# Performance work log

Hardware: AMD Instinct MI355X
Metric: run time of the kernel (lower is better)

Reference implementation:

```python
import math
import jax, jax.numpy as jnp
import numpy as np

DIM = 1024
HID = 2048  # int(dim * expansion_factor)
QK = 128
G = 256     # group size
B, N = 4, 4096
NUM_BUCKETS = 32
MAX_DIST = 128


def _rel_pos_bias(rel_emb, g, scale):
    # non-causal T5 relative position bucket (num_buckets halved to 16)
    pos = jnp.arange(g)
    rel = pos[None, :] - pos[:, None]          # k_pos - q_pos
    n = -rel
    nb = NUM_BUCKETS // 2                       # 16
    ret = (n < 0).astype(jnp.int32) * nb
    n = jnp.abs(n)
    max_exact = nb // 2                         # 8
    is_small = n < max_exact
    val_large = max_exact + (
        jnp.log(jnp.maximum(n, 1).astype(jnp.float32) / max_exact)
        / math.log(MAX_DIST / max_exact) * (nb - max_exact)
    ).astype(jnp.int32)
    val_large = jnp.minimum(val_large, nb - 1)
    bucket = ret + jnp.where(is_small, n, val_large)   # [g, g] in [0, 32)
    return rel_emb[bucket, 0] * scale                   # [g, g]


def _layernorm(x, g, b, eps=1e-5):
    mu = jnp.mean(x, axis=-1, keepdims=True)
    var = jnp.mean((x - mu) ** 2, axis=-1, keepdims=True)
    return (x - mu) * jax.lax.rsqrt(var + eps) * g + b


def setup_inputs() -> dict:
    key = jax.random.key(0)
    ks = jax.random.split(key, 8)
    return {
        "x": jax.random.normal(ks[0], (B, N, DIM), dtype=jnp.float32),
        "ln_g": jnp.ones((DIM,), jnp.float32),
        "ln_b": jnp.zeros((DIM,), jnp.float32),
        "W_h": jax.random.normal(ks[1], (DIM, 2 * HID), jnp.float32) * 0.02,
        "b_h": jnp.zeros((2 * HID,), jnp.float32),
        "W_qk": jax.random.normal(ks[2], (DIM, QK), jnp.float32) * 0.02,
        "b_qk": jnp.zeros((QK,), jnp.float32),
        "os_gamma": jax.random.normal(ks[3], (4, QK), jnp.float32) * 0.02,
        "os_beta": jnp.zeros((4, QK), jnp.float32),
        "rel_emb": jax.random.normal(ks[4], (NUM_BUCKETS, 1), jnp.float32) * 0.02,
        "W_out": jax.random.normal(ks[5], (HID, DIM), jnp.float32) * 0.02,
        "b_out": jnp.zeros((DIM,), jnp.float32),
    }


def reference(x, ln_g, ln_b, W_h, b_h, W_qk, b_qk, os_gamma, os_beta, rel_emb, W_out, b_out):
    b, n = x.shape[0], x.shape[1]
    ng = n // G
    normed = _layernorm(x, ln_g, ln_b)
    hid = jax.nn.silu(normed @ W_h + b_h)               # [b, n, 2*HID]
    v, gate = hid[..., :HID], hid[..., HID:]
    qk = jax.nn.silu(normed @ W_qk + b_qk)              # [b, n, QK]
    # OffsetScale heads=4 -> quad_q, lin_q, quad_k, lin_k
    heads = qk[..., None, :] * os_gamma + os_beta        # [b, n, 4, QK]
    quad_q, lin_q, quad_k, lin_k = [heads[..., h, :] for h in range(4)]
    # group into blocks of G
    def grp(t):
        return t.reshape(b, ng, G, t.shape[-1])
    quad_q, quad_k, lin_q, lin_k, vg = map(grp, (quad_q, quad_k, lin_q, lin_k, v))
    # quadratic (local) branch: ReLU^2 attention per group + T5 bias
    sim = jnp.einsum('bgid,bgjd->bgij', quad_q, quad_k) / G
    sim = sim + _rel_pos_bias(rel_emb, G, QK ** 0.5)
    attn = jax.nn.relu(sim) ** 2
    quad_out = jnp.einsum('bgij,bgje->bgie', attn, vg)   # [b, ng, G, HID]
    # linear (global) branch, reduced over groups (non-causal)
    lin_kv = jnp.einsum('bgnd,bgne->bde', lin_k, vg) / n
    lin_out = jnp.einsum('bde,bgnd->bgne', lin_kv, lin_q)
    out = (quad_out + lin_out).reshape(b, n, HID)
    out = gate * out
    return out @ W_out + b_out + x
```

## Files before the change

### kernel.cpp

```cpp
#include <hip/hip_runtime.h>
#include <hip/hip_bf16.h>


typedef __attribute__((ext_vector_type(8))) short short8;
typedef __attribute__((ext_vector_type(4))) float f32x4;

#define BM 128
#define BN 128
#define BK 32

struct Aux {
  const float* b1;
  const float* x;
  const float* gamma;
  const float* beta;
  const float* biastab;
  const unsigned short* a2;
  const unsigned short* bkv;
  const unsigned short* gate;
  unsigned short* o16a;
  unsigned short* o16b;
  unsigned short* o16c;
  unsigned short* o16d;
  float* o32;
};

__device__ __forceinline__ float bf2f(unsigned short u) {
  union { float f; unsigned int i; } w; w.i = ((unsigned int)u) << 16; return w.f;
}
__device__ __forceinline__ unsigned short f2bf(float f) {
  union { float f; unsigned int i; } w; w.f = f;
  unsigned int x = w.i;
  return (unsigned short)((x + 0x7FFFu + ((x >> 16) & 1u)) >> 16);
}
__device__ __forceinline__ float silu_f(float z) { return z / (1.0f + __expf(-z)); }

__device__ __forceinline__ void async_cp16(const unsigned short* g, unsigned short* l) {
  __builtin_amdgcn_global_load_lds(
      (const __attribute__((address_space(1))) void*)g,
      (__attribute__((address_space(3))) void*)l, 16, 0, 0);
}

__device__ __forceinline__ float block_sum(float v) {
  #pragma unroll
  for (int o = 32; o > 0; o >>= 1) v += __shfl_down(v, o, 64);
  __shared__ float sh[4];
  __syncthreads();
  if ((threadIdx.x & 63) == 0) sh[threadIdx.x >> 6] = v;
  __syncthreads();
  return sh[0] + sh[1] + sh[2] + sh[3];
}

__global__ __launch_bounds__(256) void ln_k(const float* __restrict__ x,
                                            const float* __restrict__ g,
                                            const float* __restrict__ b,
                                            unsigned short* __restrict__ out) {
  const int row = blockIdx.x;
  const int tid = threadIdx.x;
  const float4 xv = ((const float4*)(x + (size_t)row * 1024))[tid];
  float s = xv.x + xv.y + xv.z + xv.w;
  s = block_sum(s);
  const float mu = s * (1.0f / 1024.0f);
  const float d0 = xv.x - mu, d1 = xv.y - mu, d2 = xv.z - mu, d3 = xv.w - mu;
  float q = d0 * d0 + d1 * d1 + d2 * d2 + d3 * d3;
  q = block_sum(q);
  const float rstd = rsqrtf(q * (1.0f / 1024.0f) + 1e-5f);
  const float4 gv = ((const float4*)g)[tid];
  const float4 bv = ((const float4*)b)[tid];
  unsigned short* o = out + (size_t)row * 1024 + tid * 4;
  o[0] = f2bf(d0 * rstd * gv.x + bv.x);
  o[1] = f2bf(d1 * rstd * gv.y + bv.y);
  o[2] = f2bf(d2 * rstd * gv.z + bv.z);
  o[3] = f2bf(d3 * rstd * gv.w + bv.w);
}

__global__ __launch_bounds__(256) void tc_k(const float* __restrict__ in,
                                            unsigned short* __restrict__ out,
                                            int K, int N) {
  __shared__ unsigned short L[64][65];
  const int t = threadIdx.x;
  const int k0 = blockIdx.y * 64, n0 = blockIdx.x * 64;
  const int r = t >> 4, c4 = (t & 15) * 4;
  #pragma unroll
  for (int rr = 0; rr < 4; ++rr) {
    const int kk = rr * 16 + r;
    const float4 f = ((const float4*)(in + (size_t)(k0 + kk) * N + n0))[t & 15];
    L[kk][c4 + 0] = f2bf(f.x); L[kk][c4 + 1] = f2bf(f.y);
    L[kk][c4 + 2] = f2bf(f.z); L[kk][c4 + 3] = f2bf(f.w);
  }
  __syncthreads();
  #pragma unroll
  for (int rr = 0; rr < 4; ++rr) {
    const int nn = rr * 16 + r;
    ushort4 u;
    u.x = L[c4 + 0][nn]; u.y = L[c4 + 1][nn];
    u.z = L[c4 + 2][nn]; u.w = L[c4 + 3][nn];
    ((ushort4*)(out + (size_t)(n0 + nn) * K + k0))[t & 15] = u;
  }
}

__global__ void bias_k(const float* __restrict__ rel, float* __restrict__ tab) {
  int idx = blockIdx.x * 256 + threadIdx.x;
  if (idx >= 511) return;
  int d = idx - 255;
  int n = -d;
  int ret = (n < 0) ? 16 : 0;
  int a = (n < 0) ? -n : n;
  int bucket;
  if (a < 8) {
    bucket = ret + a;
  } else {
    float t = __logf((float)a * 0.125f) / 2.7725887298583984f * 8.0f;
    int vl = 8 + (int)t;
    if (vl > 15) vl = 15;
    bucket = ret + vl;
  }
  tab[idx] = rel[bucket] * 11.313708498984761f;
}

__global__ void kvred_k(const float* __restrict__ pkv, unsigned short* __restrict__ linkvT) {
  int i4 = blockIdx.x * 256 + threadIdx.x;
  const int b = i4 >> 16, rem = i4 & 65535;
  const float4* p = (const float4*)(pkv + (size_t)b * 1048576) + rem;
  const float4 p0 = p[0], p1 = p[65536], p2 = p[131072], p3 = p[196608];
  ushort4 u;
  u.x = f2bf((p0.x + p1.x + p2.x + p3.x) * (1.0f / 4096.0f));
  u.y = f2bf((p0.y + p1.y + p2.y + p3.y) * (1.0f / 4096.0f));
  u.z = f2bf((p0.z + p1.z + p2.z + p3.z) * (1.0f / 4096.0f));
  u.w = f2bf((p0.w + p1.w + p2.w + p3.w) * (1.0f / 4096.0f));
  ((ushort4*)(linkvT + (size_t)b * 262144))[rem] = u;
}

template<int MODE>
__global__ __launch_bounds__(256, 2) void gemm_k(
    const unsigned short* __restrict__ Ag,
    const unsigned short* __restrict__ Bg,
    int lda, int ldb, int kiters, Aux aux)
{
  __shared__ unsigned short As[BM * BK];
  __shared__ unsigned short Bs[BN * BK];

  const int tid  = threadIdx.x;
  const int lane = tid & 63;
  const int wave = tid >> 6;
  const int quad = lane >> 4;
  const int l16  = lane & 15;
  const int wm   = (wave >> 1) * 64;
  const int wn   = (wave & 1) * 64;
  const int bz   = blockIdx.z;
  const int bm   = blockIdx.y * BM;
  const int bn   = blockIdx.x * BN;

  const unsigned short* A = Ag;
  const unsigned short* B = Bg;
  if constexpr (MODE == 2) { A += (size_t)bz * 32768;  B += (size_t)bz * 32768; }
  if constexpr (MODE == 3) { A += (size_t)bz * 65536;
                             B += (size_t)(bz >> 4) * 8388608 + (size_t)(bz & 15) * 256; }
  if constexpr (MODE == 4) { const int b = bz >> 2, s = bz & 3;
                             A += (size_t)b * 524288 + (size_t)s * 1024;
                             B += (size_t)b * 8388608 + (size_t)s * 1024; }

  const unsigned short* A2 = nullptr;
  const unsigned short* B2 = nullptr;
  if constexpr (MODE == 3) {
    A2 = aux.a2 + (size_t)bz * 32768;
    B2 = aux.bkv + (size_t)(bz >> 4) * 262144;
  }

  const int srow = wave * 32 + (lane >> 2);
  const int scol = (lane & 3) * 8;
  unsigned short* lA = As + wave * 1024;
  unsigned short* lB = Bs + wave * 1024;

  const f32x4 zero = {0.f, 0.f, 0.f, 0.f};
  f32x4 acc[4][4];
  #pragma unroll
  for (int i = 0; i < 4; ++i)
    #pragma unroll
    for (int j = 0; j < 4; ++j) acc[i][j] = zero;

  for (int kt = 0; kt < kiters; ++kt) {
    const unsigned short* pa = A;
    const unsigned short* pb = B;
    int la = lda, lb = ldb, kk = kt * BK;
    if constexpr (MODE == 3) {
      if (kt >= 8) { pa = A2; pb = B2; la = 128; lb = 128; kk -= 256; }
    }

    __syncthreads();
    async_cp16(pa + (size_t)(bm + srow) * la + kk + scol, lA);
    async_cp16(pa + (size_t)(bm + srow + 16) * la + kk + scol, lA + 512);
    async_cp16(pb + (size_t)(bn + srow) * lb + kk + scol, lB);
    async_cp16(pb + (size_t)(bn + srow + 16) * lb + kk + scol, lB + 512);
    __syncthreads();

    short8 af[4], bfv[4];
    #pragma unroll
    for (int i = 0; i < 4; ++i)
      af[i] = *reinterpret_cast<const short8*>(As + (wm + i * 16 + l16) * BK + quad * 8);
    #pragma unroll
    for (int j = 0; j < 4; ++j)
      bfv[j] = *reinterpret_cast<const short8*>(Bs + (wn + j * 16 + l16) * BK + quad * 8);

    #pragma unroll
    for (int i = 0; i < 4; ++i)
      #pragma unroll
      for (int j = 0; j < 4; ++j)
        acc[i][j] = __builtin_amdgcn_mfma_f32_16x16x32_bf16(af[i], bfv[j], acc[i][j], 0, 0, 0);
  }

  #pragma unroll
  for (int i = 0; i < 4; ++i) {
    #pragma unroll
    for (int j = 0; j < 4; ++j) {
      const int row0 = bm + wm + i * 16 + quad * 4;
      const int col  = bn + wn + j * 16 + l16;
      if constexpr (MODE == 0) {
        const float bb = aux.b1[col];
        float s[4];
        #pragma unroll
        for (int r = 0; r < 4; ++r) s[r] = silu_f(acc[i][j][r] + bb);
        if (col < 2048) {
          const int b = row0 >> 12, t = row0 & 4095;
          ushort4 u; u.x = f2bf(s[0]); u.y = f2bf(s[1]); u.z = f2bf(s[2]); u.w = f2bf(s[3]);
          *(ushort4*)(aux.o16a + (size_t)b * 8388608 + (size_t)col * 4096 + t) = u;
        } else {
          #pragma unroll
          for (int r = 0; r < 4; ++r)
            aux.o16b[(size_t)(row0 + r) * 2048 + (col - 2048)] = f2bf(s[r]);
        }
      } else if constexpr (MODE == 1) {
        const float bb = aux.b1[col];
        float s[4];
        #pragma unroll
        for (int r = 0; r < 4; ++r) s[r] = silu_f(acc[i][j][r] + bb);
        #pragma unroll
        for (int r = 0; r < 4; ++r) {
          const size_t idx = (size_t)(row0 + r) * 128 + col;
          aux.o16a[idx] = f2bf(s[r] * aux.gamma[col]       + aux.beta[col]);
          aux.o16b[idx] = f2bf(s[r] * aux.gamma[128 + col] + aux.beta[128 + col]);
          aux.o16c[idx] = f2bf(s[r] * aux.gamma[256 + col] + aux.beta[256 + col]);
        }
        const int b = row0 >> 12, t = row0 & 4095;
        const float g4 = aux.gamma[384 + col], b4 = aux.beta[384 + col];
        ushort4 u;
        u.x = f2bf(s[0] * g4 + b4); u.y = f2bf(s[1] * g4 + b4);
        u.z = f2bf(s[2] * g4 + b4); u.w = f2bf(s[3] * g4 + b4);
        *(ushort4*)(aux.o16d + (size_t)b * 524288 + (size_t)col * 4096 + t) = u;
      } else if constexpr (MODE == 2) {
        #pragma unroll
        for (int r = 0; r < 4; ++r) {
          float s = acc[i][j][r] * (1.0f / 256.0f) + aux.biastab[col - (row0 + r) + 255];
          s = fmaxf(s, 0.0f);
          aux.o16a[(size_t)bz * 65536 + (size_t)(row0 + r) * 256 + col] = f2bf(s * s);
        }
      } else if constexpr (MODE == 3) {
        #pragma unroll
        for (int r = 0; r < 4; ++r) {
          const size_t idx = ((size_t)bz * 256 + row0 + r) * 2048 + col;
          aux.o16a[idx] = f2bf(acc[i][j][r] * bf2f(aux.gate[idx]));
        }
      } else if constexpr (MODE == 4) {
        float4 u; u.x = acc[i][j][0]; u.y = acc[i][j][1]; u.z = acc[i][j][2]; u.w = acc[i][j][3];
        *(float4*)(aux.o32 + (size_t)bz * 262144 + (size_t)col * 128 + row0) = u;
      } else if constexpr (MODE == 6) {
        #pragma unroll
        for (int r = 0; r < 4; ++r) {
          const size_t idx = (size_t)(row0 + r) * 1024 + col;
          aux.o32[idx] = acc[i][j][r] + aux.b1[col] + aux.x[idx];
        }
      }
    }
  }
}

extern "C" void kernel_launch(void* const* d_in, const int* in_sizes, int n_in,
                              void* d_out, int out_size, void* d_ws, size_t ws_size,
                              hipStream_t stream) {
  (void)in_sizes; (void)n_in; (void)out_size; (void)ws_size;
  const float* x     = (const float*)d_in[0];
  const float* ln_g  = (const float*)d_in[1];
  const float* ln_b  = (const float*)d_in[2];
  const float* W_h   = (const float*)d_in[3];
  const float* b_h   = (const float*)d_in[4];
  const float* W_qk  = (const float*)d_in[5];
  const float* b_qk  = (const float*)d_in[6];
  const float* osg   = (const float*)d_in[7];
  const float* osb   = (const float*)d_in[8];
  const float* rel   = (const float*)d_in[9];
  const float* W_out = (const float*)d_in[10];
  const float* b_out = (const float*)d_in[11];
  float* out = (float*)d_out;

  char* w = (char*)d_ws;
  size_t off = 0;
  auto alloc = [&](size_t bytes) { char* p = w + off; off += (bytes + 255) & ~(size_t)255; return p; };

  unsigned short* normed = (unsigned short*)alloc(16384ull * 1024 * 2);
  unsigned short* whT    = (unsigned short*)alloc(4096ull * 1024 * 2);
  unsigned short* qq     = (unsigned short*)alloc(16384ull * 128 * 2);
  unsigned short* qkk    = (unsigned short*)alloc(16384ull * 128 * 2);
  unsigned short* linkT  = (unsigned short*)alloc(4ull * 128 * 4096 * 2);
  float*          pkvT   = (float*)alloc(16ull * 2048 * 128 * 4);
  unsigned short* wqkT   = (unsigned short*)alloc(128ull * 1024 * 2);
  unsigned short* woutT  = (unsigned short*)alloc(1024ull * 2048 * 2);
  unsigned short* vT     = (unsigned short*)alloc(4ull * 2048 * 4096 * 2);
  unsigned short* gate   = (unsigned short*)alloc(16384ull * 2048 * 2);
  unsigned short* lq     = (unsigned short*)alloc(16384ull * 128 * 2);
  unsigned short* attn   = (unsigned short*)alloc(64ull * 256 * 256 * 2);
  unsigned short* linkvT = (unsigned short*)alloc(4ull * 2048 * 128 * 2);
  float*          btab   = (float*)alloc(511 * 4);
  unsigned short* gated  = (unsigned short*)w;

  tc_k<<<dim3(64, 16), 256, 0, stream>>>(W_h,   whT,   1024, 4096);
  tc_k<<<dim3(2, 16),  256, 0, stream>>>(W_qk,  wqkT,  1024, 128);
  tc_k<<<dim3(16, 32), 256, 0, stream>>>(W_out, woutT, 2048, 1024);
  bias_k<<<2, 256, 0, stream>>>(rel, btab);
  ln_k<<<16384, 256, 0, stream>>>(x, ln_g, ln_b, normed);

  Aux a0{}; a0.b1 = b_h; a0.o16a = vT; a0.o16b = gate;
  gemm_k<0><<<dim3(32, 128, 1), 256, 0, stream>>>(normed, whT, 1024, 1024, 32, a0);

  Aux a1{}; a1.b1 = b_qk; a1.gamma = osg; a1.beta = osb;
  a1.o16a = qq; a1.o16b = lq; a1.o16c = qkk; a1.o16d = linkT;
  gemm_k<1><<<dim3(1, 128, 1), 256, 0, stream>>>(normed, wqkT, 1024, 1024, 32, a1);

  Aux a2x{}; a2x.biastab = btab; a2x.o16a = attn;
  gemm_k<2><<<dim3(2, 2, 64), 256, 0, stream>>>(qq, qkk, 128, 128, 4, a2x);

  Aux a4{}; a4.o32 = pkvT;
  gemm_k<4><<<dim3(16, 1, 16), 256, 0, stream>>>(linkT, vT, 4096, 4096, 8, a4);

  kvred_k<<<1024, 256, 0, stream>>>(pkvT, linkvT);

  Aux a3{}; a3.a2 = lq; a3.bkv = linkvT; a3.gate = gate; a3.o16a = gated;
  gemm_k<3><<<dim3(16, 2, 64), 256, 0, stream>>>(attn, vT, 256, 4096, 12, a3);

  Aux a6{}; a6.b1 = b_out; a6.x = x; a6.o32 = out;
  gemm_k<6><<<dim3(8, 128, 1), 256, 0, stream>>>(gated, woutT, 2048, 2048, 64, a6);
}
```

Measured before the change: 602.1 us.

## Add 256x256-tile GEMM with 4-stage async LDS pipeline for big projections

Adds a new GEMM kernel with 256x256 output tiles, 512 threads and a 4-stage ring of global_load_lds buffers in 128 KB of dynamic LDS. It uses XOR-swizzled LDS layout and s_setprio around the MFMA bursts. The two largest GEMMs (hidden projection and output projection) now use it instead of the 128x128 kernel. The aim is more operand reuse per tile and memory latency hidden behind compute. In exchange, the grid has fewer blocks (1024 and 256), register pressure is high, and 128 KB of LDS per block may limit occupancy to one block per CU.

```diff
diff --git a/kernel.cpp b/kernel.cpp
--- a/kernel.cpp
+++ b/kernel.cpp
@@ -35,7 +35,7 @@
 }
 __device__ __forceinline__ float silu_f(float z) { return z / (1.0f + __expf(-z)); }
 
-__device__ __forceinline__ void async_cp16(const unsigned short* g, unsigned short* l) {
+__device__ __forceinline__ void async_cp16(const void* g, void* l) {
   __builtin_amdgcn_global_load_lds(
       (const __attribute__((address_space(1))) void*)g,
       (__attribute__((address_space(3))) void*)l, 16, 0, 0);
@@ -132,6 +132,121 @@
 }
 
 template<int MODE>
+__global__ __launch_bounds__(512, 2) void gemm256_k(
+    const unsigned short* __restrict__ Ag,
+    const unsigned short* __restrict__ Bg,
+    int lda, int ldb, int kiters, Aux aux)
+{
+  extern __shared__ __align__(16) char smem[];
+
+  const int tid  = threadIdx.x;
+  const int lane = tid & 63;
+  const int wave = tid >> 6;
+  const int quad = lane >> 4;
+  const int l16  = lane & 15;
+  const int wm   = (wave >> 2) * 128;
+  const int wn   = (wave & 3) * 64;
+  const int bm   = blockIdx.y * 256;
+  const int bn   = blockIdx.x * 256;
+
+  const size_t lda2 = (size_t)lda * 2;
+  const size_t ldb2 = (size_t)ldb * 2;
+
+  const int srow  = tid >> 2;
+  const int scolb = ((tid & 3) ^ ((tid >> 3) & 3)) << 4;
+  const char* gA = (const char*)Ag + (size_t)(bm + srow) * lda2 + scolb;
+  const char* gB = (const char*)Bg + (size_t)(bn + srow) * ldb2 + scolb;
+  char* laBase = smem + wave * 1024;
+
+  auto stage = [&](int tt) {
+    char* la = laBase + (tt & 3) * 32768;
+    const char* a = gA + (size_t)tt * 64;
+    const char* b = gB + (size_t)tt * 64;
+    async_cp16(a,              la);
+    async_cp16(a + 128 * lda2, la + 8192);
+    async_cp16(b,              la + 16384);
+    async_cp16(b + 128 * ldb2, la + 24576);
+  };
+
+  const f32x4 zero = {0.f, 0.f, 0.f, 0.f};
+  f32x4 acc[8][4];
+  #pragma unroll
+  for (int i = 0; i < 8; ++i)
+    #pragma unroll
+    for (int j = 0; j < 4; ++j) acc[i][j] = zero;
+
+  stage(0); stage(1); stage(2);
+
+  const int cw = (quad ^ ((l16 >> 1) & 3)) << 4;
+  const char* rdA = smem + (size_t)(wm + l16) * 64 + cw;
+  const char* rdB = smem + 16384 + (size_t)(wn + l16) * 64 + cw;
+
+  for (int t = 0; t < kiters; ++t) {
+    if (t < kiters - 2)       asm volatile("s_waitcnt vmcnt(8)" ::: "memory");
+    else if (t == kiters - 2) asm volatile("s_waitcnt vmcnt(4)" ::: "memory");
+    else                      asm volatile("s_waitcnt vmcnt(0)" ::: "memory");
+    __builtin_amdgcn_s_barrier();
+    asm volatile("" ::: "memory");
+
+    if (t + 3 < kiters) stage(t + 3);
+
+    const char* pA = rdA + (t & 3) * 32768;
+    const char* pB = rdB + (t & 3) * 32768;
+    short8 af[8], bf[4];
+    #pragma unroll
+    for (int j = 0; j < 4; ++j) bf[j] = *(const short8*)(pB + j * 1024);
+    #pragma unroll
+    for (int i = 0; i < 4; ++i) af[i] = *(const short8*)(pA + i * 1024);
+    __builtin_amdgcn_s_setprio(1);
+    #pragma unroll
+    for (int i = 0; i < 4; ++i)
+      #pragma unroll
+      for (int j = 0; j < 4; ++j)
+        acc[i][j] = __builtin_amdgcn_mfma_f32_16x16x32_bf16(af[i], bf[j], acc[i][j], 0, 0, 0);
+    __builtin_amdgcn_s_setprio(0);
+    #pragma unroll
+    for (int i = 4; i < 8; ++i) af[i] = *(const short8*)(pA + i * 1024);
+    __builtin_amdgcn_s_setprio(1);
+    #pragma unroll
+    for (int i = 4; i < 8; ++i)
+      #pragma unroll
+      for (int j = 0; j < 4; ++j)
+        acc[i][j] = __builtin_amdgcn_mfma_f32_16x16x32_bf16(af[i], bf[j], acc[i][j], 0, 0, 0);
+    __builtin_amdgcn_s_setprio(0);
+  }
+
+  #pragma unroll
+  for (int i = 0; i < 8; ++i) {
+    #pragma unroll
+    for (int j = 0; j < 4; ++j) {
+      const int row0 = bm + wm + i * 16 + quad * 4;
+      const int col  = bn + wn + j * 16 + l16;
+      if constexpr (MODE == 0) {
+        const float bb = aux.b1[col];
+        float s[4];
+        #pragma unroll
+        for (int r = 0; r < 4; ++r) s[r] = silu_f(acc[i][j][r] + bb);
+        if (bn < 2048) {
+          const int b = row0 >> 12, tt = row0 & 4095;
+          ushort4 u; u.x = f2bf(s[0]); u.y = f2bf(s[1]); u.z = f2bf(s[2]); u.w = f2bf(s[3]);
+          *(ushort4*)(aux.o16a + (size_t)b * 8388608 + (size_t)col * 4096 + tt) = u;
+        } else {
+          #pragma unroll
+          for (int r = 0; r < 4; ++r)
+            aux.o16b[(size_t)(row0 + r) * 2048 + (col - 2048)] = f2bf(s[r]);
+        }
+      } else {
+        #pragma unroll
+        for (int r = 0; r < 4; ++r) {
+          const size_t idx = (size_t)(row0 + r) * 1024 + col;
+          aux.o32[idx] = acc[i][j][r] + aux.b1[col] + aux.x[idx];
+        }
+      }
+    }
+  }
+}
+
+template<int MODE>
 __global__ __launch_bounds__(256, 2) void gemm_k(
     const unsigned short* __restrict__ Ag,
     const unsigned short* __restrict__ Bg,
@@ -215,21 +330,7 @@
     for (int j = 0; j < 4; ++j) {
       const int row0 = bm + wm + i * 16 + quad * 4;
       const int col  = bn + wn + j * 16 + l16;
-      if constexpr (MODE == 0) {
-        const float bb = aux.b1[col];
-        float s[4];
-        #pragma unroll
-        for (int r = 0; r < 4; ++r) s[r] = silu_f(acc[i][j][r] + bb);
-        if (col < 2048) {
-          const int b = row0 >> 12, t = row0 & 4095;
-          ushort4 u; u.x = f2bf(s[0]); u.y = f2bf(s[1]); u.z = f2bf(s[2]); u.w = f2bf(s[3]);
-          *(ushort4*)(aux.o16a + (size_t)b * 8388608 + (size_t)col * 4096 + t) = u;
-        } else {
-          #pragma unroll
-          for (int r = 0; r < 4; ++r)
-            aux.o16b[(size_t)(row0 + r) * 2048 + (col - 2048)] = f2bf(s[r]);
-        }
-      } else if constexpr (MODE == 1) {
+      if constexpr (MODE == 1) {
         const float bb = aux.b1[col];
         float s[4];
         #pragma unroll
@@ -263,12 +364,6 @@
       } else if constexpr (MODE == 4) {
         float4 u; u.x = acc[i][j][0]; u.y = acc[i][j][1]; u.z = acc[i][j][2]; u.w = acc[i][j][3];
         *(float4*)(aux.o32 + (size_t)bz * 262144 + (size_t)col * 128 + row0) = u;
-      } else if constexpr (MODE == 6) {
-        #pragma unroll
-        for (int r = 0; r < 4; ++r) {
-          const size_t idx = (size_t)(row0 + r) * 1024 + col;
-          aux.o32[idx] = acc[i][j][r] + aux.b1[col] + aux.x[idx];
-        }
       }
     }
   }
@@ -292,6 +387,15 @@
   const float* b_out = (const float*)d_in[11];
   float* out = (float*)d_out;
 
+  static bool attr_done = false;
+  if (!attr_done) {
+    hipFuncSetAttribute(reinterpret_cast<const void*>(gemm256_k<0>),
+                        hipFuncAttributeMaxDynamicSharedMemorySize, 131072);
+    hipFuncSetAttribute(reinterpret_cast<const void*>(gemm256_k<6>),
+                        hipFuncAttributeMaxDynamicSharedMemorySize, 131072);
+    attr_done = true;
+  }
+
   char* w = (char*)d_ws;
   size_t off = 0;
   auto alloc = [&](size_t bytes) { char* p = w + off; off += (bytes + 255) & ~(size_t)255; return p; };
@@ -319,7 +423,7 @@
   ln_k<<<16384, 256, 0, stream>>>(x, ln_g, ln_b, normed);
 
   Aux a0{}; a0.b1 = b_h; a0.o16a = vT; a0.o16b = gate;
-  gemm_k<0><<<dim3(32, 128, 1), 256, 0, stream>>>(normed, whT, 1024, 1024, 32, a0);
+  gemm256_k<0><<<dim3(16, 64), 512, 131072, stream>>>(normed, whT, 1024, 1024, 32, a0);
 
   Aux a1{}; a1.b1 = b_qk; a1.gamma = osg; a1.beta = osb;
   a1.o16a = qq; a1.o16b = lq; a1.o16c = qkk; a1.o16d = linkT;
@@ -337,5 +441,5 @@
   gemm_k<3><<<dim3(16, 2, 64), 256, 0, stream>>>(attn, vT, 256, 4096, 12, a3);
 
   Aux a6{}; a6.b1 = b_out; a6.x = x; a6.o32 = out;
-  gemm_k<6><<<dim3(8, 128, 1), 256, 0, stream>>>(gated, woutT, 2048, 2048, 64, a6);
-}
+  gemm256_k<6><<<dim3(4, 64), 512, 131072, stream>>>(gated, woutT, 2048, 2048, 64, a6);
+}
```

Measured after the change: 576.8 us. 4.2% less time.

## Replace LDS-staged GEMM with register-direct MFMA loads and XCD-aware block swizzle

Applied to the files above, without the earlier changes.

The two large GEMMs (hidden projection and output projection) move to a new kernel that loads A/B fragments straight from global memory into registers with double buffering, skipping LDS staging and the barriers that come with it. Block indices are remapped so consecutive workgroups (likely spread across XCDs) cover tiles that share rows and columns, which should improve L2 reuse. Occupancy is raised to 3 blocks per CU. The cost is that each wave now reads its own global data with no sharing through LDS, which raises L2 traffic and the chance of uncoalesced 16-byte reads.

```diff
diff --git a/kernel.cpp b/kernel.cpp
--- a/kernel.cpp
+++ b/kernel.cpp
@@ -35,7 +35,7 @@
 }
 __device__ __forceinline__ float silu_f(float z) { return z / (1.0f + __expf(-z)); }
 
-__device__ __forceinline__ void async_cp16(const unsigned short* g, unsigned short* l) {
+__device__ __forceinline__ void async_cp16(const void* g, void* l) {
   __builtin_amdgcn_global_load_lds(
       (const __attribute__((address_space(1))) void*)g,
       (__attribute__((address_space(3))) void*)l, 16, 0, 0);
@@ -132,6 +132,104 @@
 }
 
 template<int MODE>
+__global__ __launch_bounds__(256, 3) void gemmrs_k(
+    const unsigned short* __restrict__ Ag,
+    const unsigned short* __restrict__ Bg,
+    int lda, int ldb, int kiters, Aux aux)
+{
+  const int tid  = threadIdx.x;
+  const int lane = tid & 63;
+  const int wave = tid >> 6;
+  const int quad = lane >> 4;
+  const int l16  = lane & 15;
+  const int wm   = (wave >> 1) * 64;
+  const int wn   = (wave & 1) * 64;
+
+  const int L = blockIdx.x + gridDim.x * blockIdx.y;
+  const int p = L & 7;
+  const int s = L >> 3;
+  int by, bx;
+  if constexpr (MODE == 6) { by = (p + 8 * (s >> 6)) * 8 + (s & 7); bx = (s >> 3) & 7; }
+  else                     { by = p * 16 + (s & 15);                bx = s >> 4; }
+  const int bm = by * 128;
+  const int bn = bx * 128;
+
+  const unsigned lda2 = (unsigned)lda * 2u;
+  const unsigned ldb2 = (unsigned)ldb * 2u;
+  const char* pa[4];
+  const char* pb[4];
+  #pragma unroll
+  for (int i = 0; i < 4; ++i)
+    pa[i] = (const char*)Ag + (size_t)(unsigned)((bm + wm + i * 16 + l16) * lda2) + quad * 16;
+  #pragma unroll
+  for (int j = 0; j < 4; ++j)
+    pb[j] = (const char*)Bg + (size_t)(unsigned)((bn + wn + j * 16 + l16) * ldb2) + quad * 16;
+
+  const f32x4 zero = {0.f, 0.f, 0.f, 0.f};
+  f32x4 acc[4][4];
+  #pragma unroll
+  for (int i = 0; i < 4; ++i)
+    #pragma unroll
+    for (int j = 0; j < 4; ++j) acc[i][j] = zero;
+
+  short8 ca[4], cb[4], na[4], nb[4];
+
+#define LOAD8(DA, DB)                                            \
+  _Pragma("unroll")                                              \
+  for (int i = 0; i < 4; ++i) {                                  \
+    DA[i] = *(const short8*)pa[i];  pa[i] += 64;                 \
+    DB[i] = *(const short8*)pb[i];  pb[i] += 64;                 \
+  }
+#define MFMA16(SA, SB)                                           \
+  _Pragma("unroll")                                              \
+  for (int i = 0; i < 4; ++i)                                    \
+    _Pragma("unroll")                                            \
+    for (int j = 0; j < 4; ++j)                                  \
+      acc[i][j] = __builtin_amdgcn_mfma_f32_16x16x32_bf16(       \
+          SA[i], SB[j], acc[i][j], 0, 0, 0);
+
+  LOAD8(ca, cb);
+  for (int t = 0; t < kiters; t += 2) {
+    if (t + 1 < kiters) LOAD8(na, nb);
+    MFMA16(ca, cb);
+    if (t + 2 < kiters) LOAD8(ca, cb);
+    MFMA16(na, nb);
+  }
+#undef LOAD8
+#undef MFMA16
+
+  #pragma unroll
+  for (int i = 0; i < 4; ++i) {
+    #pragma unroll
+    for (int j = 0; j < 4; ++j) {
+      const int row0 = bm + wm + i * 16 + quad * 4;
+      const int col  = bn + wn + j * 16 + l16;
+      if constexpr (MODE == 0) {
+        const float bb = aux.b1[col];
+        float s4[4];
+        #pragma unroll
+        for (int r = 0; r < 4; ++r) s4[r] = silu_f(acc[i][j][r] + bb);
+        if (col < 2048) {
+          const int b = row0 >> 12, tt = row0 & 4095;
+          ushort4 u; u.x = f2bf(s4[0]); u.y = f2bf(s4[1]); u.z = f2bf(s4[2]); u.w = f2bf(s4[3]);
+          *(ushort4*)(aux.o16a + (size_t)b * 8388608 + (size_t)col * 4096 + tt) = u;
+        } else {
+          #pragma unroll
+          for (int r = 0; r < 4; ++r)
+            aux.o16b[(size_t)(row0 + r) * 2048 + (col - 2048)] = f2bf(s4[r]);
+        }
+      } else {
+        #pragma unroll
+        for (int r = 0; r < 4; ++r) {
+          const size_t idx = (size_t)(row0 + r) * 1024 + col;
+          aux.o32[idx] = acc[i][j][r] + aux.b1[col] + aux.x[idx];
+        }
+      }
+    }
+  }
+}
+
+template<int MODE>
 __global__ __launch_bounds__(256, 2) void gemm_k(
     const unsigned short* __restrict__ Ag,
     const unsigned short* __restrict__ Bg,
@@ -215,21 +313,7 @@
     for (int j = 0; j < 4; ++j) {
       const int row0 = bm + wm + i * 16 + quad * 4;
       const int col  = bn + wn + j * 16 + l16;
-      if constexpr (MODE == 0) {
-        const float bb = aux.b1[col];
-        float s[4];
-        #pragma unroll
-        for (int r = 0; r < 4; ++r) s[r] = silu_f(acc[i][j][r] + bb);
-        if (col < 2048) {
-          const int b = row0 >> 12, t = row0 & 4095;
-          ushort4 u; u.x = f2bf(s[0]); u.y = f2bf(s[1]); u.z = f2bf(s[2]); u.w = f2bf(s[3]);
-          *(ushort4*)(aux.o16a + (size_t)b * 8388608 + (size_t)col * 4096 + t) = u;
-        } else {
-          #pragma unroll
-          for (int r = 0; r < 4; ++r)
-            aux.o16b[(size_t)(row0 + r) * 2048 + (col - 2048)] = f2bf(s[r]);
-        }
-      } else if constexpr (MODE == 1) {
+      if constexpr (MODE == 1) {
         const float bb = aux.b1[col];
         float s[4];
         #pragma unroll
@@ -263,12 +347,6 @@
       } else if constexpr (MODE == 4) {
         float4 u; u.x = acc[i][j][0]; u.y = acc[i][j][1]; u.z = acc[i][j][2]; u.w = acc[i][j][3];
         *(float4*)(aux.o32 + (size_t)bz * 262144 + (size_t)col * 128 + row0) = u;
-      } else if constexpr (MODE == 6) {
-        #pragma unroll
-        for (int r = 0; r < 4; ++r) {
-          const size_t idx = (size_t)(row0 + r) * 1024 + col;
-          aux.o32[idx] = acc[i][j][r] + aux.b1[col] + aux.x[idx];
-        }
       }
     }
   }
@@ -319,7 +397,7 @@
   ln_k<<<16384, 256, 0, stream>>>(x, ln_g, ln_b, normed);
 
   Aux a0{}; a0.b1 = b_h; a0.o16a = vT; a0.o16b = gate;
-  gemm_k<0><<<dim3(32, 128, 1), 256, 0, stream>>>(normed, whT, 1024, 1024, 32, a0);
+  gemmrs_k<0><<<dim3(32, 128), 256, 0, stream>>>(normed, whT, 1024, 1024, 32, a0);
 
   Aux a1{}; a1.b1 = b_qk; a1.gamma = osg; a1.beta = osb;
   a1.o16a = qq; a1.o16b = lq; a1.o16c = qkk; a1.o16d = linkT;
@@ -337,5 +415,5 @@
   gemm_k<3><<<dim3(16, 2, 64), 256, 0, stream>>>(attn, vT, 256, 4096, 12, a3);
 
   Aux a6{}; a6.b1 = b_out; a6.x = x; a6.o32 = out;
-  gemm_k<6><<<dim3(8, 128, 1), 256, 0, stream>>>(gated, woutT, 2048, 2048, 64, a6);
-}
+  gemmrs_k<6><<<dim3(8, 128), 256, 0, stream>>>(gated, woutT, 2048, 2048, 64, a6);
+}
```

Measured after the change: 1.022 ms. 1.7x slower.
